# Kernel optimization log

Measured on AMD Instinct MI355X. Metric: run time of the kernel, lower is better.

The kernel has to match this reference:

```python
import jax, jax.numpy as jnp
import numpy as np

NUM_HEADS = 12


def setup_inputs() -> dict:
    key = jax.random.key(0)
    ks = jax.random.split(key, 5)
    B, N, C = 64, 388, 768  # N = 8*8*2 + 16*16 + 4
    return {
        "x": jax.random.normal(ks[0], (B, N, C), dtype=jnp.float32),
        "qkv_w": jax.random.normal(ks[1], (3 * C, C), dtype=jnp.float32) * 0.02,
        "qkv_b": jax.random.normal(ks[2], (3 * C,), dtype=jnp.float32) * 0.02,
        "proj_w": jax.random.normal(ks[3], (C, C), dtype=jnp.float32) * 0.02,
        "proj_b": jax.random.normal(ks[4], (C,), dtype=jnp.float32) * 0.02,
        "t_h": 8, "t_w": 8, "s_h": 16, "s_w": 16,
    }


def reference(x, qkv_w, qkv_b, proj_w, proj_b, t_h, t_w, s_h, s_w):
    B, N, C = x.shape
    H = NUM_HEADS
    D = C // H
    scale = D ** -0.5
    L_t = t_h * t_w * 2          # template (x2) tokens
    L_s = s_h * s_w + 4          # search tokens + 4 extra

    qkv = x @ qkv_w.T + qkv_b                       # [B,N,3C]
    qkv = qkv.reshape(B, N, 3, H, D).transpose(2, 0, 3, 1, 4)  # [3,B,H,N,D]
    q, k, v = qkv[0], qkv[1], qkv[2]                # each [B,H,N,D]

    q_mt, q_s = q[:, :, :L_t], q[:, :, L_t:]
    k_mt = k[:, :, :L_t]
    v_mt = v[:, :, :L_t]

    # template self-attention (template queries attend only to template keys)
    attn_mt = jax.nn.softmax(jnp.einsum("bhqd,bhkd->bhqk", q_mt, k_mt) * scale, axis=-1)
    x_mt = jnp.einsum("bhqk,bhkd->bhqd", attn_mt, v_mt)  # [B,H,L_t,D]
    x_mt = x_mt.transpose(0, 2, 1, 3).reshape(B, L_t, C)

    # search queries attend to ALL keys
    attn_s = jax.nn.softmax(jnp.einsum("bhqd,bhkd->bhqk", q_s, k) * scale, axis=-1)
    x_s = jnp.einsum("bhqk,bhkd->bhqd", attn_s, v)  # [B,H,L_s,D]
    x_s = x_s.transpose(0, 2, 1, 3).reshape(B, L_s, C)

    out = jnp.concatenate([x_mt, x_s], axis=1)      # [B,N,C]
    out = out @ proj_w.T + proj_b
    return out
```

## Files before the change

### kernel.cpp

```cpp
#include <hip/hip_runtime.h>
#include <cstdint>
#include <cstddef>
#include <cmath>

typedef __attribute__((ext_vector_type(4))) float f32x4;
typedef __attribute__((ext_vector_type(8))) short bf16x8;

typedef const __attribute__((address_space(1))) void* gas_ptr;
typedef __attribute__((address_space(3))) void* las_ptr;

static __device__ __forceinline__ short f2bf(float f) {
    __bf16 h = (__bf16)f;
    return __builtin_bit_cast(short, h);
}

constexpr int MP = 25088;

__global__ void cvt_all(const float* __restrict__ x,  const float* __restrict__ qw,
                        const float* __restrict__ pw,
                        short* __restrict__ xb, short* __restrict__ qwb,
                        short* __restrict__ pwb)
{
    constexpr int NX = MP * 768 / 4;
    constexpr int NQ = 2304 * 768 / 4;
    constexpr int NP = 768 * 768 / 4;
    constexpr int NT = NX + NQ + NP;
    int i = blockIdx.x * blockDim.x + threadIdx.x;
    const int stride = gridDim.x * blockDim.x;
    for (; i < NT; i += stride) {
        if (i < NX) {
            const int flat = i * 4;
            const int mp  = flat / 768;
            const int col = flat - mp * 768;
            const int b   = mp / 392;
            const int nn  = mp - b * 392;
            short4 o;
            if (nn < 388) {
                const float4 v = *reinterpret_cast<const float4*>(
                    x + ((size_t)(b * 388 + nn) * 768 + col));
                o.x = f2bf(v.x); o.y = f2bf(v.y); o.z = f2bf(v.z); o.w = f2bf(v.w);
            } else {
                o.x = 0; o.y = 0; o.z = 0; o.w = 0;
            }
            reinterpret_cast<short4*>(xb)[i] = o;
        } else if (i < NX + NQ) {
            const int j = i - NX;
            const float4 v = reinterpret_cast<const float4*>(qw)[j];
            short4 o;
            o.x = f2bf(v.x); o.y = f2bf(v.y); o.z = f2bf(v.z); o.w = f2bf(v.w);
            reinterpret_cast<short4*>(qwb)[j] = o;
        } else {
            const int j = i - NX - NQ;
            const float4 v = reinterpret_cast<const float4*>(pw)[j];
            short4 o;
            o.x = f2bf(v.x); o.y = f2bf(v.y); o.z = f2bf(v.z); o.w = f2bf(v.w);
            reinterpret_cast<short4*>(pwb)[j] = o;
        }
    }
}

template<int MODE>
__global__ __launch_bounds__(256) void gemm_bt(
    const short* __restrict__ A, const short* __restrict__ Bw,
    const float* __restrict__ bias,
    short* __restrict__ qk, short* __restrict__ vT,
    float* __restrict__ fo, int NB)
{
    constexpr int K = 768;
    constexpr int KT = 12;
    __shared__ __align__(16) short ldsraw[2 * 128 * 64 * 2];
    short* ldsA = ldsraw;
    short* ldsB = ldsraw + 2 * 128 * 64;

    const int tid  = threadIdx.x;
    const int lane = tid & 63;
    const int wid  = tid >> 6;
    const int lrow = lane & 15;
    const int lgrp = lane >> 4;
    const int wr   = wid >> 1;
    const int wc   = wid & 1;

    const int nwg = gridDim.x;
    const int q8  = nwg >> 3, r8 = nwg & 7;
    const int xcd = blockIdx.x & 7, bidx = blockIdx.x >> 3;
    const int wgid = (xcd < r8 ? xcd * (q8 + 1) : r8 * (q8 + 1) + (xcd - r8) * q8) + bidx;

    int m0, n0;
    if constexpr (MODE == 0) {
        constexpr int G = 14, SG = G * 18;
        const int mg = wgid / SG;
        const int r  = wgid - mg * SG;
        const int n  = r / G;
        const int mi = r - n * G;
        m0 = (mg * G + mi) * 128;
        n0 = n * 128;
    } else {
        m0 = (wgid / NB) * 128;
        n0 = (wgid % NB) * 128;
    }

    f32x4 acc[4][4];
    #pragma unroll
    for (int i = 0; i < 4; ++i)
        #pragma unroll
        for (int j = 0; j < 4; ++j)
            acc[i][j] = f32x4{0.f, 0.f, 0.f, 0.f};

    auto stage = [&](int kt, int buf) {
        #pragma unroll
        for (int it = 0; it < 4; ++it) {
            const int c   = it * 256 + wid * 64 + lane;
            const int row = c >> 3;
            const int scb = ((c & 7) * 16) ^ ((row & 7) << 4);
            const short* ga = A  + (size_t)(m0 + row) * K + kt * 64 + (scb >> 1);
            const short* gb = Bw + (size_t)(n0 + row) * K + kt * 64 + (scb >> 1);
            __builtin_amdgcn_global_load_lds((gas_ptr)ga, (las_ptr)((char*)(ldsA + buf * 128 * 64) + c * 16), 16, 0, 0);
            __builtin_amdgcn_global_load_lds((gas_ptr)gb, (las_ptr)((char*)(ldsB + buf * 128 * 64) + c * 16), 16, 0, 0);
        }
    };

    stage(0, 0);

    for (int kt = 0; kt < KT; ++kt) {
        const int cur = kt & 1;
        if (kt + 1 < KT) {
            stage(kt + 1, cur ^ 1);
            asm volatile("s_waitcnt vmcnt(8)" ::: "memory");
        } else {
            asm volatile("s_waitcnt vmcnt(0)" ::: "memory");
        }
        __builtin_amdgcn_s_barrier();
        __builtin_amdgcn_sched_barrier(0);

        #pragma unroll
        for (int ks = 0; ks < 2; ++ks) {
            bf16x8 af[4], bfv[4];
            #pragma unroll
            for (int i = 0; i < 4; ++i) {
                const int r   = wr * 64 + i * 16 + lrow;
                const int byt = r * 128 + ((ks * 64 + lgrp * 16) ^ ((r & 7) << 4));
                af[i] = *reinterpret_cast<const bf16x8*>((const char*)(ldsA + cur * 128 * 64) + byt);
            }
            #pragma unroll
            for (int j = 0; j < 4; ++j) {
                const int r   = wc * 64 + j * 16 + lrow;
                const int byt = r * 128 + ((ks * 64 + lgrp * 16) ^ ((r & 7) << 4));
                bfv[j] = *reinterpret_cast<const bf16x8*>((const char*)(ldsB + cur * 128 * 64) + byt);
            }
            #pragma unroll
            for (int i = 0; i < 4; ++i)
                #pragma unroll
                for (int j = 0; j < 4; ++j)
                    acc[i][j] = __builtin_amdgcn_mfma_f32_16x16x32_bf16(af[i], bfv[j], acc[i][j], 0, 0, 0);
        }

        __builtin_amdgcn_sched_barrier(0);
        __builtin_amdgcn_s_barrier();
    }

    const int mb = m0 + wr * 64;
    const int nb = n0 + wc * 64;
    if constexpr (MODE == 0) {
        if (n0 < 1536) {
            #pragma unroll
            for (int j = 0; j < 4; ++j) {
                const int c  = nb + j * 16 + lrow;
                const float sc = (c < 768) ? 0.18033688011116f : 1.0f;
                const float bv = bias[c];
                #pragma unroll
                for (int i = 0; i < 4; ++i) {
                    #pragma unroll
                    for (int r = 0; r < 4; ++r) {
                        const int m = mb + i * 16 + lgrp * 4 + r;
                        qk[(size_t)m * 1536 + c] = f2bf((acc[i][j][r] + bv) * sc);
                    }
                }
            }
        } else {
            const int h = (nb - 1536) >> 6;
            short* lw = ldsraw + wid * (64 * 80);
            #pragma unroll
            for (int j = 0; j < 4; ++j) {
                const int dloc = j * 16 + lrow;
                const float bv = bias[nb + j * 16 + lrow];
                #pragma unroll
                for (int i = 0; i < 4; ++i)
                    #pragma unroll
                    for (int r = 0; r < 4; ++r)
                        lw[dloc * 80 + i * 16 + lgrp * 4 + r] = f2bf(acc[i][j][r] + bv);
            }
            asm volatile("s_waitcnt lgkmcnt(0)" ::: "memory");
            __builtin_amdgcn_sched_barrier(0);
            #pragma unroll
            for (int w = 0; w < 8; ++w) {
                const int d    = w * 8 + (lane >> 3);
                const int nloc = (lane & 7) * 8;
                const bf16x8 val = *reinterpret_cast<const bf16x8*>(lw + d * 80 + nloc);
                const int mchunk = mb + nloc;
                const int b  = mchunk / 392;
                const int nn = mchunk - b * 392;
                short* dst = vT + ((size_t)(b * 12 + h) * 64 + d) * 392 + nn;
                *reinterpret_cast<bf16x8*>(dst) = val;
            }
        }
    } else {
        #pragma unroll
        for (int i = 0; i < 4; ++i) {
            #pragma unroll
            for (int r = 0; r < 4; ++r) {
                const int m = mb + i * 16 + lgrp * 4 + r;
                #pragma unroll
                for (int j = 0; j < 4; ++j) {
                    const int c = nb + j * 16 + lrow;
                    fo[(size_t)m * 768 + c] = acc[i][j][r] + bias[c];
                }
            }
        }
    }
}

constexpr int PSTRB = 128;

static __device__ __forceinline__ void attn_chunk64(
    int kbeg, int k_len,
    const short* __restrict__ klds, const short* __restrict__ vlds,
    const bf16x8 (&qf)[2], char* __restrict__ my,
    int lrow, int lgrp,
    float& rs, f32x4 (&oacc)[4])
{
    f32x4 sacc[4];
    #pragma unroll
    for (int t = 0; t < 4; ++t) sacc[t] = f32x4{0.f, 0.f, 0.f, 0.f};

    #pragma unroll
    for (int t = 0; t < 4; ++t) {
        const int kl   = t * 16 + lrow;
        const int byt0 = kl * 128 + ((lgrp * 16) ^ ((kl & 7) << 4));
        const int byt1 = kl * 128 + ((64 + lgrp * 16) ^ ((kl & 7) << 4));
        const bf16x8 k0 = *reinterpret_cast<const bf16x8*>((const char*)klds + byt0);
        const bf16x8 k1 = *reinterpret_cast<const bf16x8*>((const char*)klds + byt1);
        sacc[t] = __builtin_amdgcn_mfma_f32_16x16x32_bf16(k0, qf[0], sacc[t], 0, 0, 0);
        sacc[t] = __builtin_amdgcn_mfma_f32_16x16x32_bf16(k1, qf[1], sacc[t], 0, 0, 0);
    }

    if (kbeg + 64 <= k_len) {
        #pragma unroll
        for (int t = 0; t < 4; ++t) {
            short4 pk;
            #pragma unroll
            for (int r = 0; r < 4; ++r) {
                const float p = exp2f(sacc[t][r]);
                rs += p;
                ((short*)&pk)[r] = f2bf(p);
            }
            const int byt = lrow * PSTRB + ((t * 32 + lgrp * 8) ^ ((lrow & 7) << 4));
            *reinterpret_cast<short4*>(my + byt) = pk;
        }
    } else {
        #pragma unroll
        for (int t = 0; t < 4; ++t) {
            short4 pk;
            #pragma unroll
            for (int r = 0; r < 4; ++r) {
                const int key = kbeg + t * 16 + lgrp * 4 + r;
                const float p = (key < k_len) ? exp2f(sacc[t][r]) : 0.f;
                rs += p;
                ((short*)&pk)[r] = f2bf(p);
            }
            const int byt = lrow * PSTRB + ((t * 32 + lgrp * 8) ^ ((lrow & 7) << 4));
            *reinterpret_cast<short4*>(my + byt) = pk;
        }
    }

    #pragma unroll
    for (int ks = 0; ks < 2; ++ks) {
        const bf16x8 pf = *reinterpret_cast<const bf16x8*>(
            my + lrow * PSTRB + ((ks * 64 + lgrp * 16) ^ ((lrow & 7) << 4)));
        #pragma unroll
        for (int dt = 0; dt < 4; ++dt) {
            const int d = dt * 16 + lrow;
            const bf16x8 vf = *reinterpret_cast<const bf16x8*>(
                (const char*)vlds + d * 128 + ((ks * 64 + lgrp * 16) ^ ((d & 7) << 4)));
            oacc[dt] = __builtin_amdgcn_mfma_f32_16x16x32_bf16(pf, vf, oacc[dt], 0, 0, 0);
        }
    }
}

__global__ __launch_bounds__(256, 4) void attn_flash(
    const short* __restrict__ qkb, const short* __restrict__ vT,
    short* __restrict__ ao)
{
    __shared__ __align__(16) short klds[2][64 * 64];
    __shared__ __align__(16) short vlds[2][64 * 64];
    __shared__ __align__(16) char  plds[4][16 * PSTRB];

    const int tid  = threadIdx.x;
    const int lane = tid & 63;
    const int wid  = tid >> 6;
    const int lrow = lane & 15;
    const int lgrp = lane >> 4;

    const int blk = blockIdx.x;
    const int xcd = blk & 7;
    const int i7  = blk >> 3;
    const int bh  = xcd * 96 + i7 / 7;
    const int bx  = i7 % 7;

    int q_start, qend, k_len, nch;
    if (bx < 2) { q_start = bx * 64;             qend = 128; k_len = 128; nch = 2; }
    else        { q_start = 128 + (bx - 2) * 64; qend = 388; k_len = 388; nch = 7; }

    const int q0 = q_start + wid * 16;

    const int b = bh / 12, h = bh - b * 12;
    const short* qbase = qkb + (size_t)b * 392 * 1536 + h * 64;
    const short* kbase = qbase + 768;
    const short* vbase = vT + (size_t)bh * 64 * 392;

    int qrow = q0 + lrow; if (qrow >= qend) qrow = qend - 1;
    bf16x8 qf[2];
    #pragma unroll
    for (int ks = 0; ks < 2; ++ks)
        qf[ks] = *reinterpret_cast<const bf16x8*>(qbase + (size_t)qrow * 1536 + ks * 32 + lgrp * 8);

    float rs = 0.f;
    f32x4 oacc[4];
    #pragma unroll
    for (int dt = 0; dt < 4; ++dt) oacc[dt] = f32x4{0.f, 0.f, 0.f, 0.f};

    char* my = &plds[wid][0];

    auto stage64 = [&](int ch, int buf) {
        const int kbeg = ch * 64;
        #pragma unroll
        for (int it = 0; it < 2; ++it) {
            const int c = it * 256 + tid;
            const int krow = c >> 3;
            const int scb = ((c & 7) * 16) ^ ((krow & 7) << 4);
            int g = kbeg + krow; if (g > 391) g = 391;
            const short* gk = kbase + (size_t)g * 1536 + (scb >> 1);
            __builtin_amdgcn_global_load_lds((gas_ptr)gk, (las_ptr)((char*)&klds[buf][0] + c * 16), 16, 0, 0);
        }
        #pragma unroll
        for (int it = 0; it < 2; ++it) {
            const int c = it * 256 + tid;
            const int vrow = c >> 3;
            const int scb = ((c & 7) * 16) ^ ((vrow & 7) << 4);
            const short* gv = vbase + (size_t)vrow * 392 + kbeg + (scb >> 1);
            __builtin_amdgcn_global_load_lds((gas_ptr)gv, (las_ptr)((char*)&vlds[buf][0] + c * 16), 16, 0, 0);
        }
    };

    stage64(0, 0);

    for (int ch = 0; ch < nch; ++ch) {
        const int cur = ch & 1;
        if (ch + 1 < nch) {
            stage64(ch + 1, cur ^ 1);
            asm volatile("s_waitcnt vmcnt(4)" ::: "memory");
        } else {
            asm volatile("s_waitcnt vmcnt(0)" ::: "memory");
        }
        __builtin_amdgcn_s_barrier();
        __builtin_amdgcn_sched_barrier(0);

        attn_chunk64(ch * 64, k_len, &klds[cur][0], &vlds[cur][0],
                     qf, my, lrow, lgrp, rs, oacc);

        __builtin_amdgcn_sched_barrier(0);
        __builtin_amdgcn_s_barrier();
    }

    rs += __shfl_xor(rs, 16, 64);
    rs += __shfl_xor(rs, 32, 64);

    float inv[4];
    #pragma unroll
    for (int r = 0; r < 4; ++r) inv[r] = 1.0f / __shfl(rs, lgrp * 4 + r, 64);

    #pragma unroll
    for (int r = 0; r < 4; ++r) {
        const int qn = q0 + lgrp * 4 + r;
        if (qn < qend) {
            #pragma unroll
            for (int dt = 0; dt < 4; ++dt)
                ao[((size_t)b * 388 + qn) * 768 + h * 64 + dt * 16 + lrow] =
                    f2bf(oacc[dt][r] * inv[r]);
        }
    }
}

extern "C" void kernel_launch(void* const* d_in, const int* in_sizes, int n_in,
                              void* d_out, int out_size, void* d_ws, size_t ws_size,
                              hipStream_t stream) {
    (void)in_sizes; (void)n_in; (void)out_size; (void)ws_size;
    const float* x      = (const float*)d_in[0];
    const float* qkv_w  = (const float*)d_in[1];
    const float* qkv_b  = (const float*)d_in[2];
    const float* proj_w = (const float*)d_in[3];
    const float* proj_b = (const float*)d_in[4];
    float* out = (float*)d_out;

    char* ws = (char*)d_ws;
    short* xb   = (short*)(ws);
    short* attn = (short*)(ws);
    short* qkb  = (short*)(ws + 38535168);
    short* vTb  = (short*)(ws + 115605504);
    short* qwb  = (short*)(ws + 154140672);
    short* pwb  = (short*)(ws + 157679616);

    cvt_all<<<2048, 256, 0, stream>>>(x, qkv_w, proj_w, xb, qwb, pwb);

    gemm_bt<0><<<dim3(196 * 18), 256, 0, stream>>>(xb, qwb, qkv_b, qkb, vTb, nullptr, 18);

    attn_flash<<<dim3(5376), 256, 0, stream>>>(qkb, vTb, attn);

    gemm_bt<1><<<dim3(194 * 6), 256, 0, stream>>>(attn, pwb, proj_b, nullptr, nullptr, out, 6);
}
```

Before: 221.4 us.

## Fuse fp32-to-bf16 conversion of x into the QKV GEMM A-tile load

Drops the separate pass that converted x to a padded bf16 buffer. The QKV GEMM now reads fp32 x directly through registers, converts each value to bf16 and writes it into swizzled LDS, with padding rows clamped to the last valid token. This removes one full write and read of the bf16 copy of x. In exchange, the A tile is staged through registers instead of async global_load_lds, and the fp32 reads are twice as large. Each of the 18 N-tile blocks also re-reads and re-converts the same A data, which may raise register pressure and reduce load/compute overlap.

```diff
diff --git a/kernel.cpp b/kernel.cpp
--- a/kernel.cpp
+++ b/kernel.cpp
@@ -16,41 +16,22 @@
 
 constexpr int MP = 25088;
 
-__global__ void cvt_all(const float* __restrict__ x,  const float* __restrict__ qw,
-                        const float* __restrict__ pw,
-                        short* __restrict__ xb, short* __restrict__ qwb,
-                        short* __restrict__ pwb)
+__global__ void cvt_w(const float* __restrict__ qw, const float* __restrict__ pw,
+                      short* __restrict__ qwb, short* __restrict__ pwb)
 {
-    constexpr int NX = MP * 768 / 4;
     constexpr int NQ = 2304 * 768 / 4;
     constexpr int NP = 768 * 768 / 4;
-    constexpr int NT = NX + NQ + NP;
+    constexpr int NT = NQ + NP;
     int i = blockIdx.x * blockDim.x + threadIdx.x;
     const int stride = gridDim.x * blockDim.x;
     for (; i < NT; i += stride) {
-        if (i < NX) {
-            const int flat = i * 4;
-            const int mp  = flat / 768;
-            const int col = flat - mp * 768;
-            const int b   = mp / 392;
-            const int nn  = mp - b * 392;
-            short4 o;
-            if (nn < 388) {
-                const float4 v = *reinterpret_cast<const float4*>(
-                    x + ((size_t)(b * 388 + nn) * 768 + col));
-                o.x = f2bf(v.x); o.y = f2bf(v.y); o.z = f2bf(v.z); o.w = f2bf(v.w);
-            } else {
-                o.x = 0; o.y = 0; o.z = 0; o.w = 0;
-            }
-            reinterpret_cast<short4*>(xb)[i] = o;
-        } else if (i < NX + NQ) {
-            const int j = i - NX;
-            const float4 v = reinterpret_cast<const float4*>(qw)[j];
+        if (i < NQ) {
+            const float4 v = reinterpret_cast<const float4*>(qw)[i];
             short4 o;
             o.x = f2bf(v.x); o.y = f2bf(v.y); o.z = f2bf(v.z); o.w = f2bf(v.w);
-            reinterpret_cast<short4*>(qwb)[j] = o;
+            reinterpret_cast<short4*>(qwb)[i] = o;
         } else {
-            const int j = i - NX - NQ;
+            const int j = i - NQ;
             const float4 v = reinterpret_cast<const float4*>(pw)[j];
             short4 o;
             o.x = f2bf(v.x); o.y = f2bf(v.y); o.z = f2bf(v.z); o.w = f2bf(v.w);
@@ -59,12 +40,10 @@
     }
 }
 
-template<int MODE>
-__global__ __launch_bounds__(256) void gemm_bt(
-    const short* __restrict__ A, const short* __restrict__ Bw,
+__global__ __launch_bounds__(256) void gemm_qkv(
+    const float* __restrict__ X, const short* __restrict__ Bw,
     const float* __restrict__ bias,
-    short* __restrict__ qk, short* __restrict__ vT,
-    float* __restrict__ fo, int NB)
+    short* __restrict__ qk, short* __restrict__ vT)
 {
     constexpr int K = 768;
     constexpr int KT = 12;
@@ -85,19 +64,180 @@
     const int xcd = blockIdx.x & 7, bidx = blockIdx.x >> 3;
     const int wgid = (xcd < r8 ? xcd * (q8 + 1) : r8 * (q8 + 1) + (xcd - r8) * q8) + bidx;
 
-    int m0, n0;
-    if constexpr (MODE == 0) {
-        constexpr int G = 14, SG = G * 18;
-        const int mg = wgid / SG;
-        const int r  = wgid - mg * SG;
-        const int n  = r / G;
-        const int mi = r - n * G;
-        m0 = (mg * G + mi) * 128;
-        n0 = n * 128;
+    constexpr int G = 14, SG = G * 18;
+    const int mg = wgid / SG;
+    const int r_ = wgid - mg * SG;
+    const int n_ = r_ / G;
+    const int mi = r_ - n_ * G;
+    const int m0 = (mg * G + mi) * 128;
+    const int n0 = n_ * 128;
+
+    f32x4 acc[4][4];
+    #pragma unroll
+    for (int i = 0; i < 4; ++i)
+        #pragma unroll
+        for (int j = 0; j < 4; ++j)
+            acc[i][j] = f32x4{0.f, 0.f, 0.f, 0.f};
+
+    const float* abase[4];
+    #pragma unroll
+    for (int it = 0; it < 4; ++it) {
+        const int c   = it * 256 + tid;
+        const int row = c >> 3;
+        const int scb = ((c & 7) * 16) ^ ((row & 7) << 4);
+        const int kcol = scb >> 1;
+        const int mp = m0 + row;
+        const int b  = mp / 392;
+        int nn = mp - b * 392; if (nn > 387) nn = 387;
+        abase[it] = X + (size_t)(b * 388 + nn) * 768 + kcol;
+    }
+
+    float4 ar[4][2];
+    auto loadA = [&](int kt) {
+        #pragma unroll
+        for (int it = 0; it < 4; ++it) {
+            ar[it][0] = *reinterpret_cast<const float4*>(abase[it] + kt * 64);
+            ar[it][1] = *reinterpret_cast<const float4*>(abase[it] + kt * 64 + 4);
+        }
+    };
+    auto writeA = [&](int buf) {
+        #pragma unroll
+        for (int it = 0; it < 4; ++it) {
+            const int c = it * 256 + tid;
+            bf16x8 v;
+            v[0] = f2bf(ar[it][0].x); v[1] = f2bf(ar[it][0].y);
+            v[2] = f2bf(ar[it][0].z); v[3] = f2bf(ar[it][0].w);
+            v[4] = f2bf(ar[it][1].x); v[5] = f2bf(ar[it][1].y);
+            v[6] = f2bf(ar[it][1].z); v[7] = f2bf(ar[it][1].w);
+            *reinterpret_cast<bf16x8*>((char*)(ldsA + buf * 128 * 64) + c * 16) = v;
+        }
+    };
+    auto stageB = [&](int kt, int buf) {
+        #pragma unroll
+        for (int it = 0; it < 4; ++it) {
+            const int c   = it * 256 + wid * 64 + lane;
+            const int row = c >> 3;
+            const int scb = ((c & 7) * 16) ^ ((row & 7) << 4);
+            const short* gb = Bw + (size_t)(n0 + row) * K + kt * 64 + (scb >> 1);
+            __builtin_amdgcn_global_load_lds((gas_ptr)gb, (las_ptr)((char*)(ldsB + buf * 128 * 64) + c * 16), 16, 0, 0);
+        }
+    };
+
+    loadA(0);
+    stageB(0, 0);
+    writeA(0);
+    asm volatile("s_waitcnt vmcnt(0)" ::: "memory");
+    asm volatile("s_waitcnt lgkmcnt(0)" ::: "memory");
+    __builtin_amdgcn_s_barrier();
+
+    for (int kt = 0; kt < KT; ++kt) {
+        const int cur = kt & 1;
+        const bool more = (kt + 1 < KT);
+        if (more) {
+            loadA(kt + 1);
+            stageB(kt + 1, cur ^ 1);
+        }
+
+        #pragma unroll
+        for (int ks = 0; ks < 2; ++ks) {
+            bf16x8 af[4], bfv[4];
+            #pragma unroll
+            for (int i = 0; i < 4; ++i) {
+                const int r   = wr * 64 + i * 16 + lrow;
+                const int byt = r * 128 + ((ks * 64 + lgrp * 16) ^ ((r & 7) << 4));
+                af[i] = *reinterpret_cast<const bf16x8*>((const char*)(ldsA + cur * 128 * 64) + byt);
+            }
+            #pragma unroll
+            for (int j = 0; j < 4; ++j) {
+                const int r   = wc * 64 + j * 16 + lrow;
+                const int byt = r * 128 + ((ks * 64 + lgrp * 16) ^ ((r & 7) << 4));
+                bfv[j] = *reinterpret_cast<const bf16x8*>((const char*)(ldsB + cur * 128 * 64) + byt);
+            }
+            #pragma unroll
+            for (int i = 0; i < 4; ++i)
+                #pragma unroll
+                for (int j = 0; j < 4; ++j)
+                    acc[i][j] = __builtin_amdgcn_mfma_f32_16x16x32_bf16(af[i], bfv[j], acc[i][j], 0, 0, 0);
+        }
+
+        if (more) writeA(cur ^ 1);
+
+        __builtin_amdgcn_sched_barrier(0);
+        asm volatile("s_waitcnt vmcnt(0)" ::: "memory");
+        asm volatile("s_waitcnt lgkmcnt(0)" ::: "memory");
+        __builtin_amdgcn_s_barrier();
+    }
+
+    const int mb = m0 + wr * 64;
+    const int nb = n0 + wc * 64;
+    if (n0 < 1536) {
+        #pragma unroll
+        for (int j = 0; j < 4; ++j) {
+            const int c  = nb + j * 16 + lrow;
+            const float sc = (c < 768) ? 0.18033688011116f : 1.0f;
+            const float bv = bias[c];
+            #pragma unroll
+            for (int i = 0; i < 4; ++i) {
+                #pragma unroll
+                for (int r = 0; r < 4; ++r) {
+                    const int m = mb + i * 16 + lgrp * 4 + r;
+                    qk[(size_t)m * 1536 + c] = f2bf((acc[i][j][r] + bv) * sc);
+                }
+            }
+        }
     } else {
-        m0 = (wgid / NB) * 128;
-        n0 = (wgid % NB) * 128;
-    }
+        const int h = (nb - 1536) >> 6;
+        short* lw = ldsraw + wid * (64 * 80);
+        #pragma unroll
+        for (int j = 0; j < 4; ++j) {
+            const int dloc = j * 16 + lrow;
+            const float bv = bias[nb + j * 16 + lrow];
+            #pragma unroll
+            for (int i = 0; i < 4; ++i)
+                #pragma unroll
+                for (int r = 0; r < 4; ++r)
+                    lw[dloc * 80 + i * 16 + lgrp * 4 + r] = f2bf(acc[i][j][r] + bv);
+        }
+        asm volatile("s_waitcnt lgkmcnt(0)" ::: "memory");
+        __builtin_amdgcn_sched_barrier(0);
+        #pragma unroll
+        for (int w = 0; w < 8; ++w) {
+            const int d    = w * 8 + (lane >> 3);
+            const int nloc = (lane & 7) * 8;
+            const bf16x8 val = *reinterpret_cast<const bf16x8*>(lw + d * 80 + nloc);
+            const int mchunk = mb + nloc;
+            const int b  = mchunk / 392;
+            const int nn = mchunk - b * 392;
+            short* dst = vT + ((size_t)(b * 12 + h) * 64 + d) * 392 + nn;
+            *reinterpret_cast<bf16x8*>(dst) = val;
+        }
+    }
+}
+
+__global__ __launch_bounds__(256) void gemm_proj(
+    const short* __restrict__ A, const short* __restrict__ Bw,
+    const float* __restrict__ bias, float* __restrict__ fo, int NB)
+{
+    constexpr int K = 768;
+    constexpr int KT = 12;
+    __shared__ __align__(16) short ldsraw[2 * 128 * 64 * 2];
+    short* ldsA = ldsraw;
+    short* ldsB = ldsraw + 2 * 128 * 64;
+
+    const int tid  = threadIdx.x;
+    const int lane = tid & 63;
+    const int wid  = tid >> 6;
+    const int lrow = lane & 15;
+    const int lgrp = lane >> 4;
+    const int wr   = wid >> 1;
+    const int wc   = wid & 1;
+
+    const int nwg = gridDim.x;
+    const int q8  = nwg >> 3, r8 = nwg & 7;
+    const int xcd = blockIdx.x & 7, bidx = blockIdx.x >> 3;
+    const int wgid = (xcd < r8 ? xcd * (q8 + 1) : r8 * (q8 + 1) + (xcd - r8) * q8) + bidx;
+    const int m0 = (wgid / NB) * 128;
+    const int n0 = (wgid % NB) * 128;
 
     f32x4 acc[4][4];
     #pragma unroll
@@ -160,60 +300,15 @@
 
     const int mb = m0 + wr * 64;
     const int nb = n0 + wc * 64;
-    if constexpr (MODE == 0) {
-        if (n0 < 1536) {
+    #pragma unroll
+    for (int i = 0; i < 4; ++i) {
+        #pragma unroll
+        for (int r = 0; r < 4; ++r) {
+            const int m = mb + i * 16 + lgrp * 4 + r;
             #pragma unroll
             for (int j = 0; j < 4; ++j) {
-                const int c  = nb + j * 16 + lrow;
-                const float sc = (c < 768) ? 0.18033688011116f : 1.0f;
-                const float bv = bias[c];
-                #pragma unroll
-                for (int i = 0; i < 4; ++i) {
-                    #pragma unroll
-                    for (int r = 0; r < 4; ++r) {
-                        const int m = mb + i * 16 + lgrp * 4 + r;
-                        qk[(size_t)m * 1536 + c] = f2bf((acc[i][j][r] + bv) * sc);
-                    }
-                }
-            }
-        } else {
-            const int h = (nb - 1536) >> 6;
-            short* lw = ldsraw + wid * (64 * 80);
-            #pragma unroll
-            for (int j = 0; j < 4; ++j) {
-                const int dloc = j * 16 + lrow;
-                const float bv = bias[nb + j * 16 + lrow];
-                #pragma unroll
-                for (int i = 0; i < 4; ++i)
-                    #pragma unroll
-                    for (int r = 0; r < 4; ++r)
-                        lw[dloc * 80 + i * 16 + lgrp * 4 + r] = f2bf(acc[i][j][r] + bv);
-            }
-            asm volatile("s_waitcnt lgkmcnt(0)" ::: "memory");
-            __builtin_amdgcn_sched_barrier(0);
-            #pragma unroll
-            for (int w = 0; w < 8; ++w) {
-                const int d    = w * 8 + (lane >> 3);
-                const int nloc = (lane & 7) * 8;
-                const bf16x8 val = *reinterpret_cast<const bf16x8*>(lw + d * 80 + nloc);
-                const int mchunk = mb + nloc;
-                const int b  = mchunk / 392;
-                const int nn = mchunk - b * 392;
-                short* dst = vT + ((size_t)(b * 12 + h) * 64 + d) * 392 + nn;
-                *reinterpret_cast<bf16x8*>(dst) = val;
-            }
-        }
-    } else {
-        #pragma unroll
-        for (int i = 0; i < 4; ++i) {
-            #pragma unroll
-            for (int r = 0; r < 4; ++r) {
-                const int m = mb + i * 16 + lgrp * 4 + r;
-                #pragma unroll
-                for (int j = 0; j < 4; ++j) {
-                    const int c = nb + j * 16 + lrow;
-                    fo[(size_t)m * 768 + c] = acc[i][j][r] + bias[c];
-                }
+                const int c = nb + j * 16 + lrow;
+                fo[(size_t)m * 768 + c] = acc[i][j][r] + bias[c];
             }
         }
     }
@@ -402,18 +497,17 @@
     float* out = (float*)d_out;
 
     char* ws = (char*)d_ws;
-    short* xb   = (short*)(ws);
     short* attn = (short*)(ws);
     short* qkb  = (short*)(ws + 38535168);
     short* vTb  = (short*)(ws + 115605504);
     short* qwb  = (short*)(ws + 154140672);
     short* pwb  = (short*)(ws + 157679616);
 
-    cvt_all<<<2048, 256, 0, stream>>>(x, qkv_w, proj_w, xb, qwb, pwb);
-
-    gemm_bt<0><<<dim3(196 * 18), 256, 0, stream>>>(xb, qwb, qkv_b, qkb, vTb, nullptr, 18);
+    cvt_w<<<1024, 256, 0, stream>>>(qkv_w, proj_w, qwb, pwb);
+
+    gemm_qkv<<<dim3(196 * 18), 256, 0, stream>>>(x, qwb, qkv_b, qkb, vTb);
 
     attn_flash<<<dim3(5376), 256, 0, stream>>>(qkb, vTb, attn);
 
-    gemm_bt<1><<<dim3(194 * 6), 256, 0, stream>>>(attn, pwb, proj_b, nullptr, nullptr, out, 6);
-}
+    gemm_proj<<<dim3(194 * 6), 256, 0, stream>>>(attn, pwb, proj_b, out, 6);
+}
```

New measurement: 289.1 us. +30.6%, slower.

## Use 256x256 tiles with 8 waves for the QKV projection GEMM

Applied to the files above, without the earlier changes.

Replaces the 128x128 QKV GEMM with a dedicated kernel using 256x256 output tiles, 512 threads (8 waves, each computing 128x64) and double-buffered LDS of 128KB. This raises arithmetic intensity per LDS/global load and cuts the grid from 3528 to 882 workgroups. The V-transpose epilogue now runs in two passes. The tradeoff is higher register pressure (32 accumulators per thread), fewer waves per CU from the larger LDS footprint, and a smaller grid that may leave tail imbalance across CUs.

```diff
diff --git a/kernel.cpp b/kernel.cpp
--- a/kernel.cpp
+++ b/kernel.cpp
@@ -59,12 +59,150 @@
     }
 }
 
-template<int MODE>
-__global__ __launch_bounds__(256) void gemm_bt(
+__global__ __launch_bounds__(512, 2) void gemm_qkv256(
     const short* __restrict__ A, const short* __restrict__ Bw,
     const float* __restrict__ bias,
-    short* __restrict__ qk, short* __restrict__ vT,
-    float* __restrict__ fo, int NB)
+    short* __restrict__ qk, short* __restrict__ vT)
+{
+    constexpr int K = 768;
+    constexpr int KT = 12;
+    __shared__ __align__(16) short lds[2][2][256 * 64];
+
+    const int tid  = threadIdx.x;
+    const int lane = tid & 63;
+    const int wid  = tid >> 6;
+    const int lrow = lane & 15;
+    const int lgrp = lane >> 4;
+    const int wr   = wid >> 2;
+    const int wc   = wid & 3;
+
+    const int nwg = gridDim.x;
+    const int q8  = nwg >> 3, r8 = nwg & 7;
+    const int xcd = blockIdx.x & 7, bidx = blockIdx.x >> 3;
+    const int wgid = (xcd < r8 ? xcd * (q8 + 1) : r8 * (q8 + 1) + (xcd - r8) * q8) + bidx;
+    constexpr int G = 14, SG = G * 9;
+    const int mg  = wgid / SG;
+    const int r_  = wgid - mg * SG;
+    const int nn_ = r_ / G;
+    const int mi  = r_ - nn_ * G;
+    const int m0  = (mg * G + mi) * 256;
+    const int n0  = nn_ * 256;
+
+    f32x4 acc[8][4];
+    #pragma unroll
+    for (int i = 0; i < 8; ++i)
+        #pragma unroll
+        for (int j = 0; j < 4; ++j)
+            acc[i][j] = f32x4{0.f, 0.f, 0.f, 0.f};
+
+    auto stage = [&](int kt, int buf) {
+        #pragma unroll
+        for (int it = 0; it < 4; ++it) {
+            const int c   = it * 512 + tid;
+            const int row = c >> 3;
+            const int scb = ((c & 7) * 16) ^ ((row & 7) << 4);
+            const short* ga = A  + (size_t)(m0 + row) * K + kt * 64 + (scb >> 1);
+            const short* gb = Bw + (size_t)(n0 + row) * K + kt * 64 + (scb >> 1);
+            __builtin_amdgcn_global_load_lds((gas_ptr)ga, (las_ptr)((char*)&lds[buf][0][0] + c * 16), 16, 0, 0);
+            __builtin_amdgcn_global_load_lds((gas_ptr)gb, (las_ptr)((char*)&lds[buf][1][0] + c * 16), 16, 0, 0);
+        }
+    };
+
+    stage(0, 0);
+
+    for (int kt = 0; kt < KT; ++kt) {
+        const int cur = kt & 1;
+        if (kt + 1 < KT) {
+            stage(kt + 1, cur ^ 1);
+            asm volatile("s_waitcnt vmcnt(8)" ::: "memory");
+        } else {
+            asm volatile("s_waitcnt vmcnt(0)" ::: "memory");
+        }
+        __builtin_amdgcn_s_barrier();
+        __builtin_amdgcn_sched_barrier(0);
+
+        #pragma unroll
+        for (int ks = 0; ks < 2; ++ks) {
+            bf16x8 af[8], bfv[4];
+            #pragma unroll
+            for (int i = 0; i < 8; ++i) {
+                const int r   = wr * 128 + i * 16 + lrow;
+                const int byt = r * 128 + ((ks * 64 + lgrp * 16) ^ ((r & 7) << 4));
+                af[i] = *reinterpret_cast<const bf16x8*>((const char*)&lds[cur][0][0] + byt);
+            }
+            #pragma unroll
+            for (int j = 0; j < 4; ++j) {
+                const int r   = wc * 64 + j * 16 + lrow;
+                const int byt = r * 128 + ((ks * 64 + lgrp * 16) ^ ((r & 7) << 4));
+                bfv[j] = *reinterpret_cast<const bf16x8*>((const char*)&lds[cur][1][0] + byt);
+            }
+            #pragma unroll
+            for (int i = 0; i < 8; ++i)
+                #pragma unroll
+                for (int j = 0; j < 4; ++j)
+                    acc[i][j] = __builtin_amdgcn_mfma_f32_16x16x32_bf16(af[i], bfv[j], acc[i][j], 0, 0, 0);
+        }
+
+        __builtin_amdgcn_sched_barrier(0);
+        __builtin_amdgcn_s_barrier();
+    }
+
+    const int mb = m0 + wr * 128;
+    const int nb = n0 + wc * 64;
+    if (n0 < 1536) {
+        #pragma unroll
+        for (int j = 0; j < 4; ++j) {
+            const int c  = nb + j * 16 + lrow;
+            const float sc = (c < 768) ? 0.18033688011116f : 1.0f;
+            const float bv = bias[c];
+            #pragma unroll
+            for (int i = 0; i < 8; ++i) {
+                #pragma unroll
+                for (int r = 0; r < 4; ++r) {
+                    const int m = mb + i * 16 + lgrp * 4 + r;
+                    qk[(size_t)m * 1536 + c] = f2bf((acc[i][j][r] + bv) * sc);
+                }
+            }
+        }
+    } else {
+        const int h = (nb - 1536) >> 6;
+        short* lw = (short*)&lds[0][0][0] + wid * (64 * 80);
+        #pragma unroll
+        for (int pass = 0; pass < 2; ++pass) {
+            if (pass) {
+                asm volatile("s_waitcnt lgkmcnt(0)" ::: "memory");
+                __builtin_amdgcn_sched_barrier(0);
+            }
+            #pragma unroll
+            for (int j = 0; j < 4; ++j) {
+                const int dloc = j * 16 + lrow;
+                const float bv = bias[nb + j * 16 + lrow];
+                #pragma unroll
+                for (int ii = 0; ii < 4; ++ii)
+                    #pragma unroll
+                    for (int r = 0; r < 4; ++r)
+                        lw[dloc * 80 + ii * 16 + lgrp * 4 + r] = f2bf(acc[pass * 4 + ii][j][r] + bv);
+            }
+            asm volatile("s_waitcnt lgkmcnt(0)" ::: "memory");
+            __builtin_amdgcn_sched_barrier(0);
+            #pragma unroll
+            for (int w = 0; w < 8; ++w) {
+                const int d    = w * 8 + (lane >> 3);
+                const int nloc = (lane & 7) * 8;
+                const bf16x8 val = *reinterpret_cast<const bf16x8*>(lw + d * 80 + nloc);
+                const int mchunk = mb + pass * 64 + nloc;
+                const int b  = mchunk / 392;
+                const int nn = mchunk - b * 392;
+                short* dst = vT + ((size_t)(b * 12 + h) * 64 + d) * 392 + nn;
+                *reinterpret_cast<bf16x8*>(dst) = val;
+            }
+        }
+    }
+}
+
+__global__ __launch_bounds__(256) void gemm_proj(
+    const short* __restrict__ A, const short* __restrict__ Bw,
+    const float* __restrict__ bias, float* __restrict__ fo, int NB)
 {
     constexpr int K = 768;
     constexpr int KT = 12;
@@ -84,20 +222,8 @@
     const int q8  = nwg >> 3, r8 = nwg & 7;
     const int xcd = blockIdx.x & 7, bidx = blockIdx.x >> 3;
     const int wgid = (xcd < r8 ? xcd * (q8 + 1) : r8 * (q8 + 1) + (xcd - r8) * q8) + bidx;
-
-    int m0, n0;
-    if constexpr (MODE == 0) {
-        constexpr int G = 14, SG = G * 18;
-        const int mg = wgid / SG;
-        const int r  = wgid - mg * SG;
-        const int n  = r / G;
-        const int mi = r - n * G;
-        m0 = (mg * G + mi) * 128;
-        n0 = n * 128;
-    } else {
-        m0 = (wgid / NB) * 128;
-        n0 = (wgid % NB) * 128;
-    }
+    const int m0 = (wgid / NB) * 128;
+    const int n0 = (wgid % NB) * 128;
 
     f32x4 acc[4][4];
     #pragma unroll
@@ -160,60 +286,15 @@
 
     const int mb = m0 + wr * 64;
     const int nb = n0 + wc * 64;
-    if constexpr (MODE == 0) {
-        if (n0 < 1536) {
+    #pragma unroll
+    for (int i = 0; i < 4; ++i) {
+        #pragma unroll
+        for (int r = 0; r < 4; ++r) {
+            const int m = mb + i * 16 + lgrp * 4 + r;
             #pragma unroll
             for (int j = 0; j < 4; ++j) {
-                const int c  = nb + j * 16 + lrow;
-                const float sc = (c < 768) ? 0.18033688011116f : 1.0f;
-                const float bv = bias[c];
-                #pragma unroll
-                for (int i = 0; i < 4; ++i) {
-                    #pragma unroll
-                    for (int r = 0; r < 4; ++r) {
-                        const int m = mb + i * 16 + lgrp * 4 + r;
-                        qk[(size_t)m * 1536 + c] = f2bf((acc[i][j][r] + bv) * sc);
-                    }
-                }
-            }
-        } else {
-            const int h = (nb - 1536) >> 6;
-            short* lw = ldsraw + wid * (64 * 80);
-            #pragma unroll
-            for (int j = 0; j < 4; ++j) {
-                const int dloc = j * 16 + lrow;
-                const float bv = bias[nb + j * 16 + lrow];
-                #pragma unroll
-                for (int i = 0; i < 4; ++i)
-                    #pragma unroll
-                    for (int r = 0; r < 4; ++r)
-                        lw[dloc * 80 + i * 16 + lgrp * 4 + r] = f2bf(acc[i][j][r] + bv);
-            }
-            asm volatile("s_waitcnt lgkmcnt(0)" ::: "memory");
-            __builtin_amdgcn_sched_barrier(0);
-            #pragma unroll
-            for (int w = 0; w < 8; ++w) {
-                const int d    = w * 8 + (lane >> 3);
-                const int nloc = (lane & 7) * 8;
-                const bf16x8 val = *reinterpret_cast<const bf16x8*>(lw + d * 80 + nloc);
-                const int mchunk = mb + nloc;
-                const int b  = mchunk / 392;
-                const int nn = mchunk - b * 392;
-                short* dst = vT + ((size_t)(b * 12 + h) * 64 + d) * 392 + nn;
-                *reinterpret_cast<bf16x8*>(dst) = val;
-            }
-        }
-    } else {
-        #pragma unroll
-        for (int i = 0; i < 4; ++i) {
-            #pragma unroll
-            for (int r = 0; r < 4; ++r) {
-                const int m = mb + i * 16 + lgrp * 4 + r;
-                #pragma unroll
-                for (int j = 0; j < 4; ++j) {
-                    const int c = nb + j * 16 + lrow;
-                    fo[(size_t)m * 768 + c] = acc[i][j][r] + bias[c];
-                }
+                const int c = nb + j * 16 + lrow;
+                fo[(size_t)m * 768 + c] = acc[i][j][r] + bias[c];
             }
         }
     }
@@ -411,9 +492,9 @@
 
     cvt_all<<<2048, 256, 0, stream>>>(x, qkv_w, proj_w, xb, qwb, pwb);
 
-    gemm_bt<0><<<dim3(196 * 18), 256, 0, stream>>>(xb, qwb, qkv_b, qkb, vTb, nullptr, 18);
+    gemm_qkv256<<<dim3(98 * 9), 512, 0, stream>>>(xb, qwb, qkv_b, qkb, vTb);
 
     attn_flash<<<dim3(5376), 256, 0, stream>>>(qkb, vTb, attn);
 
-    gemm_bt<1><<<dim3(194 * 6), 256, 0, stream>>>(attn, pwb, proj_b, nullptr, nullptr, out, 6);
-}
+    gemm_proj<<<dim3(194 * 6), 256, 0, stream>>>(attn, pwb, proj_b, out, 6);
+}
```

Measured after the change: 229.9 us. +3.9%, slower.
